# Kernel tuning notes

Measured on AMD Instinct MI355X. Metric: run time of the kernel, lower is better.

The kernel has to match this reference:

```python
import jax, jax.numpy as jnp
import numpy as np

NEG_SLOPE = 0.01  # torch LeakyReLU default

def setup_inputs() -> dict:
    key = jax.random.key(0)
    ks = jax.random.split(key, 8)
    B, T, D = 8, 2048, 512
    E, H = 8, 2 * D  # n_experts, ffn hidden
    s = 0.02
    return {
        "x":  jax.random.normal(ks[0], (B, T, D), dtype=jnp.float32),
        "Wr": jax.random.normal(ks[1], (D, E), dtype=jnp.float32) * s,
        "br": jnp.zeros((E,), dtype=jnp.float32),
        "W1": jax.random.normal(ks[2], (E, D, H), dtype=jnp.float32) * s,
        "b1": jnp.zeros((E, H), dtype=jnp.float32),
        "W2": jax.random.normal(ks[3], (E, H, D), dtype=jnp.float32) * s,
        "b2": jnp.zeros((E, D), dtype=jnp.float32),
    }

def reference(x, Wr, br, W1, b1, W2, b2):
    B, T, D = x.shape
    E = Wr.shape[1]
    top_k = 2
    balancing_coef = 1e-4
    x_flat = x.reshape(B * T, D)  # [N, D]

    # router: softmax over experts
    router_probs = jax.nn.softmax(x_flat @ Wr + br, axis=-1)  # [N, E]
    top_weights, top_indices = jax.lax.top_k(router_probs, top_k)  # [N, k]

    # dense all-expert FFN (faithful to original: every expert on every token)
    h = jax.nn.leaky_relu(jnp.einsum('nd,edh->neh', x_flat, W1) + b1, NEG_SLOPE)  # [N, E, H]
    expert_out = jax.nn.leaky_relu(jnp.einsum('neh,ehd->ned', h, W2) + b2, NEG_SLOPE)  # [N, E, D]
    # dropout is identity in eval mode

    # gather top-k expert outputs and combine with router weights
    top_out = jnp.take_along_axis(expert_out, top_indices[:, :, None], axis=1)  # [N, k, D]
    out_flat = jnp.sum(top_out * top_weights[:, :, None], axis=1)  # [N, D]
    output = out_flat.reshape(B, T, D)

    # load-balancing loss
    target = jnp.full((E,), 1.0 / E, dtype=x.dtype)
    mean_probs = jnp.mean(router_probs, axis=0)
    gating_loss = jnp.mean((target - mean_probs) ** 2) * balancing_coef
    return (output, gating_loss)
```

## Files before the change

### kernel.cpp

```cpp
#include <hip/hip_runtime.h>
#include <hip/hip_bf16.h>

constexpr int D_    = 512;
constexpr int H_    = 1024;
constexpr int E_    = 8;
constexpr int NTOK_ = 16384;
constexpr int MT_   = 64;
constexpr int NPAIR_= 2*NTOK_;
constexpr float NEG_ = 0.01f;

typedef short s16x8 __attribute__((ext_vector_type(8)));
typedef float f32x4 __attribute__((ext_vector_type(4)));

#define MFMA16(a,b,c) __builtin_amdgcn_mfma_f32_16x16x32_bf16((a),(b),(c),0,0,0)

__device__ __forceinline__ unsigned short f2bf(float f) {
  unsigned u = __float_as_uint(f);
  u += 0x7FFFu + ((u >> 16) & 1u);
  return (unsigned short)(u >> 16);
}
__device__ __forceinline__ float bf2f(unsigned u16) {
  return __uint_as_float(u16 << 16);
}
__device__ __forceinline__ float leaky(float v) {
  return v > 0.f ? v : NEG_ * v;
}

__global__ __launch_bounds__(256) void prep_kernel(
    const float* __restrict__ x, const float* __restrict__ Wr,
    const float* __restrict__ br,
    const float* __restrict__ W1, const float* __restrict__ W2,
    unsigned short* __restrict__ W1s, unsigned short* __restrict__ W2s,
    int* __restrict__ cnt, float* __restrict__ psum,
    int* __restrict__ tokE, int* __restrict__ tokSlot, float* __restrict__ tokW) {
  const int blk = blockIdx.x;
  const int tid = threadIdx.x;
  if (blk < 64) {
    __shared__ int lcnt[E_];
    __shared__ int gbase[E_];
    __shared__ float lp[E_];
    if (tid < E_) { lcnt[tid] = 0; lp[tid] = 0.f; }
    __syncthreads();

    int t = blk * 256 + tid;
    float acc[E_];
#pragma unroll
    for (int e = 0; e < E_; e++) acc[e] = br[e];
    const float4* xr = (const float4*)(x + (size_t)t * D_);
    for (int i = 0; i < D_ / 4; i++) {
      float4 v = xr[i];
      const float* w = Wr + (size_t)i * 4 * E_;
#pragma unroll
      for (int e = 0; e < E_; e++)
        acc[e] += v.x * w[e] + v.y * w[8 + e] + v.z * w[16 + e] + v.w * w[24 + e];
    }
    float mx = acc[0];
#pragma unroll
    for (int e = 1; e < E_; e++) mx = fmaxf(mx, acc[e]);
    float p[E_]; float s = 0.f;
#pragma unroll
    for (int e = 0; e < E_; e++) { p[e] = expf(acc[e] - mx); s += p[e]; }
    float inv = 1.f / s;
#pragma unroll
    for (int e = 0; e < E_; e++) p[e] *= inv;

    float m1 = -1.f, m2 = -1.f; int i1 = 0, i2 = 0;
#pragma unroll
    for (int e = 0; e < E_; e++) {
      float pe = p[e];
      if (pe > m1)      { m2 = m1; i2 = i1; m1 = pe; i1 = e; }
      else if (pe > m2) { m2 = pe; i2 = e; }
    }
    int s1 = atomicAdd(&lcnt[i1], 1);
    int s2 = atomicAdd(&lcnt[i2], 1);

#pragma unroll
    for (int e = 0; e < E_; e++) {
      float v = p[e];
#pragma unroll
      for (int o = 32; o > 0; o >>= 1) v += __shfl_xor(v, o);
      if ((tid & 63) == 0) atomicAdd(&lp[e], v);
    }
    __syncthreads();
    if (tid < E_) {
      gbase[tid] = atomicAdd(&cnt[tid * 16], lcnt[tid]);
      atomicAdd(&psum[tid * 16], lp[tid]);
    }
    __syncthreads();
    tokE[2 * t]     = i1; tokSlot[2 * t]     = gbase[i1] + s1; tokW[2 * t]     = m1;
    tokE[2 * t + 1] = i2; tokSlot[2 * t + 1] = gbase[i2] + s2; tokW[2 * t + 1] = m2;
  } else {
    int gid = (blk - 64) * 256 + tid;
    const int HALF = E_ * 64 * 16 * 64;
    if (gid < HALF) {
      int lane = gid & 63, kk = (gid >> 6) & 15, nt = (gid >> 10) & 63, e = gid >> 16;
      int k0 = kk * 32 + (lane >> 4) * 8;
      int n  = nt * 16 + (lane & 15);
      const float* src = W1 + ((size_t)(e * 512 + k0)) * 1024 + n;
      s16x8 v;
#pragma unroll
      for (int j = 0; j < 8; j++) v[j] = (short)f2bf(src[(size_t)j * 1024]);
      *(s16x8*)(W1s + (size_t)gid * 8) = v;
    } else {
      int c = gid - HALF;
      int lane = c & 63, kk = (c >> 6) & 31, nt = (c >> 11) & 31, e = c >> 16;
      int k0 = kk * 32 + (lane >> 4) * 8;
      int n  = nt * 16 + (lane & 15);
      const float* src = W2 + ((size_t)(e * 1024 + k0)) * 512 + n;
      s16x8 v;
#pragma unroll
      for (int j = 0; j < 8; j++) v[j] = (short)f2bf(src[(size_t)j * 512]);
      *(s16x8*)(W2s + (size_t)c * 8) = v;
    }
  }
}

__global__ __launch_bounds__(256) void assign_kernel(
    const int* __restrict__ tokE, const int* __restrict__ tokSlot,
    const int* __restrict__ cnt, const float* __restrict__ psum,
    int* __restrict__ posOfTok, int* __restrict__ tokOfPos,
    float* __restrict__ loss_out) {
  __shared__ int soff[E_];
  int tid = threadIdx.x;
  if (tid == 0) {
    int o = 0;
#pragma unroll
    for (int e = 0; e < E_; e++) { soff[e] = o; o += cnt[e * 16]; }
  }
  __syncthreads();
  int p = blockIdx.x * 256 + tid;
  int pos = soff[tokE[p]] + tokSlot[p];
  posOfTok[p] = pos;
  tokOfPos[pos] = p >> 1;
  if (blockIdx.x == 0 && tid == 0) {
    float l = 0.f;
#pragma unroll
    for (int e = 0; e < E_; e++) {
      float d = 0.125f - psum[e * 16] / (float)NTOK_;
      l += d * d;
    }
    *loss_out = (l / 8.f) * 1e-4f;
  }
}

__global__ __launch_bounds__(512, 2) void ffn_kernel(
    const float* __restrict__ x,
    const unsigned short* __restrict__ W1s, const unsigned short* __restrict__ W2s,
    const float* __restrict__ b1, const float* __restrict__ b2,
    const int* __restrict__ cnt, const int* __restrict__ tokOfPos,
    unsigned short* __restrict__ buf) {
  const int e = blockIdx.x & 7;
  const int tile = blockIdx.x >> 3;
  int nTok = 0, base0 = 0;
#pragma unroll
  for (int i = 0; i < E_; i++) {
    int ci = cnt[i * 16];
    if (i < e) base0 += ci;
    if (i == e) nTok = ci;
  }
  const int start = tile * MT_;
  if (start >= nTok) return;
  const int valid = min(MT_, nTok - start);
  const int base = base0 + start;

  __shared__ __align__(16) unsigned short xs[MT_][D_ + 8];
  __shared__ __align__(16) unsigned short hs[MT_][D_ + 8];

  const int tid = threadIdx.x;
  const int w = tid >> 6;
  const int lane = tid & 63;

  for (int r = w; r < MT_; r += 8) {
    int tok = tokOfPos[base + min(r, valid - 1)];
    const float4* src = (const float4*)(x + (size_t)tok * D_);
    float4 a = src[lane * 2], b = src[lane * 2 + 1];
    s16x8 v;
    v[0] = (short)f2bf(a.x); v[1] = (short)f2bf(a.y);
    v[2] = (short)f2bf(a.z); v[3] = (short)f2bf(a.w);
    v[4] = (short)f2bf(b.x); v[5] = (short)f2bf(b.y);
    v[6] = (short)f2bf(b.z); v[7] = (short)f2bf(b.w);
    *(s16x8*)&xs[r][lane * 8] = v;
  }
  __syncthreads();

  const int qm = lane & 15;
  const int qk = (lane >> 4) * 8;
  const int qr = (lane >> 4) * 4;

  f32x4 acc2[4][4];
#pragma unroll
  for (int mi = 0; mi < 4; mi++)
#pragma unroll
    for (int ni = 0; ni < 4; ni++) acc2[mi][ni] = {0.f, 0.f, 0.f, 0.f};

  const unsigned short* B1w = W1s + ((size_t)(e * 64 + w * 4) * 16) * 512 + lane * 8;
  const unsigned short* B2w = W2s + ((size_t)(e * 32 + w * 4) * 32) * 512 + lane * 8;

  for (int c = 0; c < 2; c++) {
    f32x4 acc1[4][4];
#pragma unroll
    for (int mi = 0; mi < 4; mi++)
#pragma unroll
      for (int ni = 0; ni < 4; ni++) acc1[mi][ni] = {0.f, 0.f, 0.f, 0.f};

    const unsigned short* B1c = B1w + (size_t)(c * 32 * 16) * 512;
#pragma unroll 4
    for (int kk = 0; kk < 16; kk++) {
      s16x8 bf[4], af[4];
#pragma unroll
      for (int ni = 0; ni < 4; ni++)
        bf[ni] = *(const s16x8*)(B1c + (size_t)(ni * 16 + kk) * 512);
#pragma unroll
      for (int mi = 0; mi < 4; mi++)
        af[mi] = *(const s16x8*)&xs[mi * 16 + qm][kk * 32 + qk];
#pragma unroll
      for (int ni = 0; ni < 4; ni++)
#pragma unroll
        for (int mi = 0; mi < 4; mi++)
          acc1[mi][ni] = MFMA16(af[mi], bf[ni], acc1[mi][ni]);
    }
    __syncthreads();
#pragma unroll
    for (int ni = 0; ni < 4; ni++) {
      int hcol = w * 64 + ni * 16 + qm;
      float bb = b1[e * H_ + c * 512 + hcol];
#pragma unroll
      for (int mi = 0; mi < 4; mi++)
#pragma unroll
        for (int r4 = 0; r4 < 4; r4++)
          hs[mi * 16 + qr + r4][hcol] = f2bf(leaky(acc1[mi][ni][r4] + bb));
    }
    __syncthreads();
    const unsigned short* B2c = B2w + (size_t)(c * 16) * 512;
#pragma unroll 4
    for (int kk = 0; kk < 16; kk++) {
      s16x8 bf[4], af[4];
#pragma unroll
      for (int ni = 0; ni < 4; ni++)
        bf[ni] = *(const s16x8*)(B2c + (size_t)(ni * 32 + kk) * 512);
#pragma unroll
      for (int mi = 0; mi < 4; mi++)
        af[mi] = *(const s16x8*)&hs[mi * 16 + qm][kk * 32 + qk];
#pragma unroll
      for (int ni = 0; ni < 4; ni++)
#pragma unroll
        for (int mi = 0; mi < 4; mi++)
          acc2[mi][ni] = MFMA16(af[mi], bf[ni], acc2[mi][ni]);
    }
  }

#pragma unroll
  for (int mi = 0; mi < 4; mi++) {
#pragma unroll
    for (int r4 = 0; r4 < 4; r4++) {
      int row = mi * 16 + qr + r4;
      if (row < valid) {
        size_t rowbase = (size_t)(base + row) * D_;
#pragma unroll
        for (int ni = 0; ni < 4; ni++) {
          int col = w * 64 + ni * 16 + qm;
          float v = leaky(acc2[mi][ni][r4] + b2[e * D_ + col]);
          buf[rowbase + col] = f2bf(v);
        }
      }
    }
  }
}

__global__ __launch_bounds__(256) void combine_kernel(
    const unsigned short* __restrict__ buf, const int* __restrict__ posOfTok,
    const float* __restrict__ tokW, float* __restrict__ out) {
  int t = blockIdx.x * 4 + (threadIdx.x >> 6);
  int lane = threadIdx.x & 63;
  int p0 = posOfTok[2 * t], p1 = posOfTok[2 * t + 1];
  float w0 = tokW[2 * t], w1 = tokW[2 * t + 1];
  uint4 u0 = ((const uint4*)(buf + (size_t)p0 * D_))[lane];
  uint4 u1 = ((const uint4*)(buf + (size_t)p1 * D_))[lane];
  float4 oA, oB;
  oA.x = w0 * bf2f(u0.x & 0xFFFFu) + w1 * bf2f(u1.x & 0xFFFFu);
  oA.y = w0 * bf2f(u0.x >> 16)     + w1 * bf2f(u1.x >> 16);
  oA.z = w0 * bf2f(u0.y & 0xFFFFu) + w1 * bf2f(u1.y & 0xFFFFu);
  oA.w = w0 * bf2f(u0.y >> 16)     + w1 * bf2f(u1.y >> 16);
  oB.x = w0 * bf2f(u0.z & 0xFFFFu) + w1 * bf2f(u1.z & 0xFFFFu);
  oB.y = w0 * bf2f(u0.z >> 16)     + w1 * bf2f(u1.z >> 16);
  oB.z = w0 * bf2f(u0.w & 0xFFFFu) + w1 * bf2f(u1.w & 0xFFFFu);
  oB.w = w0 * bf2f(u0.w >> 16)     + w1 * bf2f(u1.w >> 16);
  float4* dst = (float4*)(out + (size_t)t * D_);
  dst[lane * 2]     = oA;
  dst[lane * 2 + 1] = oB;
}

extern "C" void kernel_launch(void* const* d_in, const int* in_sizes, int n_in,
                              void* d_out, int out_size, void* d_ws, size_t ws_size,
                              hipStream_t stream) {
  const float* x  = (const float*)d_in[0];
  const float* Wr = (const float*)d_in[1];
  const float* br = (const float*)d_in[2];
  const float* W1 = (const float*)d_in[3];
  const float* b1 = (const float*)d_in[4];
  const float* W2 = (const float*)d_in[5];
  const float* b2 = (const float*)d_in[6];
  float* out = (float*)d_out;

  char* ws = (char*)d_ws;
  int*   cnt      = (int*)(ws + 0);
  float* psum     = (float*)(ws + 512);
  int*   tokE     = (int*)(ws + 4096);
  int*   tokSlot  = (int*)(ws + 4096 + 1 * 131072);
  float* tokW     = (float*)(ws + 4096 + 2 * 131072);
  int*   posOfTok = (int*)(ws + 4096 + 3 * 131072);
  int*   tokOfPos = (int*)(ws + 4096 + 4 * 131072);
  unsigned short* W1s = (unsigned short*)(ws + (1u << 20));
  unsigned short* W2s = (unsigned short*)(ws + (1u << 20) + 16777216u);
  unsigned short* buf = (unsigned short*)(ws + (1u << 20) + 33554432u);

  hipMemsetAsync(d_ws, 0, 2048, stream);
  prep_kernel<<<4160, 256, 0, stream>>>(x, Wr, br, W1, W2, W1s, W2s,
                                        cnt, psum, tokE, tokSlot, tokW);
  assign_kernel<<<NPAIR_ / 256, 256, 0, stream>>>(tokE, tokSlot, cnt, psum,
                                                  posOfTok, tokOfPos,
                                                  out + (size_t)NTOK_ * D_);
  ffn_kernel<<<(NTOK_ / MT_) * E_, 512, 0, stream>>>(x, W1s, W2s, b1, b2,
                                                     cnt, tokOfPos, buf);
  combine_kernel<<<NTOK_ / 4, 256, 0, stream>>>(buf, posOfTok, tokW, out);
}
```

Measured before the change: 298.4 us.

## Stage weight conversion through LDS and double-buffer MFMA operand loads

The weight pre-pack in prep_kernel now reads 64x64 fp32 tiles with coalesced float4 loads into shared memory and then transposes them into the MFMA-fragment bf16 layout. Before, each thread made eight strided scalar global reads. Separately, both GEMM loops in ffn_kernel now prefetch operands two k-steps ahead into register double buffers, and the bias loads and the first W2 fragments are hoisted ahead of the barrier. The aim is to hide global and LDS latency, at the cost of higher register pressure and a possible drop in occupancy.

```diff
diff --git a/kernel.cpp b/kernel.cpp
--- a/kernel.cpp
+++ b/kernel.cpp
@@ -90,27 +90,45 @@
     tokE[2 * t]     = i1; tokSlot[2 * t]     = gbase[i1] + s1; tokW[2 * t]     = m1;
     tokE[2 * t + 1] = i2; tokSlot[2 * t + 1] = gbase[i2] + s2; tokW[2 * t + 1] = m2;
   } else {
-    int gid = (blk - 64) * 256 + tid;
-    const int HALF = E_ * 64 * 16 * 64;
-    if (gid < HALF) {
-      int lane = gid & 63, kk = (gid >> 6) & 15, nt = (gid >> 10) & 63, e = gid >> 16;
-      int k0 = kk * 32 + (lane >> 4) * 8;
+    __shared__ float ldsf[64][68];
+    int bid = blk - 64;
+    const float* src;
+    int e, kt, tc, srcStride;
+    bool isW1 = bid < 1024;
+    if (isW1) {
+      e = bid >> 7; kt = (bid >> 4) & 7; tc = bid & 15; srcStride = 1024;
+      src = W1 + ((size_t)(e * 512 + kt * 64)) * 1024 + tc * 64;
+    } else {
+      int b2 = bid - 1024;
+      e = b2 >> 7; kt = (b2 >> 3) & 15; tc = b2 & 7; srcStride = 512;
+      src = W2 + ((size_t)(e * 1024 + kt * 64)) * 512 + tc * 64;
+    }
+#pragma unroll
+    for (int rep = 0; rep < 4; rep++) {
+      int row = rep * 16 + (tid >> 4);
+      int c4  = (tid & 15) * 4;
+      float4 v = *(const float4*)(src + (size_t)row * srcStride + c4);
+      ldsf[row][c4] = v.x; ldsf[row][c4 + 1] = v.y;
+      ldsf[row][c4 + 2] = v.z; ldsf[row][c4 + 3] = v.w;
+    }
+    __syncthreads();
+    int wv = tid >> 6, lane = tid & 63;
+#pragma unroll
+    for (int qi = 0; qi < 2; qi++) {
+      int q = wv * 2 + qi;
+      int ks = q >> 2, nt = q & 3;
+      int k0 = ks * 32 + (lane >> 4) * 8;
       int n  = nt * 16 + (lane & 15);
-      const float* src = W1 + ((size_t)(e * 512 + k0)) * 1024 + n;
       s16x8 v;
 #pragma unroll
-      for (int j = 0; j < 8; j++) v[j] = (short)f2bf(src[(size_t)j * 1024]);
-      *(s16x8*)(W1s + (size_t)gid * 8) = v;
-    } else {
-      int c = gid - HALF;
-      int lane = c & 63, kk = (c >> 6) & 31, nt = (c >> 11) & 31, e = c >> 16;
-      int k0 = kk * 32 + (lane >> 4) * 8;
-      int n  = nt * 16 + (lane & 15);
-      const float* src = W2 + ((size_t)(e * 1024 + k0)) * 512 + n;
-      s16x8 v;
-#pragma unroll
-      for (int j = 0; j < 8; j++) v[j] = (short)f2bf(src[(size_t)j * 512]);
-      *(s16x8*)(W2s + (size_t)c * 8) = v;
+      for (int j = 0; j < 8; j++) v[j] = (short)f2bf(ldsf[k0 + j][n]);
+      if (isW1) {
+        int ntg = tc * 4 + nt, kkg = kt * 2 + ks;
+        *(s16x8*)(W1s + (((size_t)e << 16) + (ntg << 10) + (kkg << 6) + lane) * 8) = v;
+      } else {
+        int ntg = tc * 4 + nt, kkg = kt * 2 + ks;
+        *(s16x8*)(W2s + (((size_t)e << 16) + (ntg << 11) + (kkg << 6) + lane) * 8) = v;
+      }
     }
   }
 }
@@ -204,48 +222,89 @@
       for (int ni = 0; ni < 4; ni++) acc1[mi][ni] = {0.f, 0.f, 0.f, 0.f};
 
     const unsigned short* B1c = B1w + (size_t)(c * 32 * 16) * 512;
-#pragma unroll 4
+    float bb[4];
+#pragma unroll
+    for (int ni = 0; ni < 4; ni++)
+      bb[ni] = b1[e * H_ + c * 512 + w * 64 + ni * 16 + qm];
+
+    s16x8 bfp[2][4], afp[2][4];
+#pragma unroll
+    for (int s = 0; s < 2; s++) {
+#pragma unroll
+      for (int ni = 0; ni < 4; ni++)
+        bfp[s][ni] = *(const s16x8*)(B1c + (size_t)(ni * 16 + s) * 512);
+#pragma unroll
+      for (int mi = 0; mi < 4; mi++)
+        afp[s][mi] = *(const s16x8*)&xs[mi * 16 + qm][s * 32 + qk];
+    }
+#pragma unroll
     for (int kk = 0; kk < 16; kk++) {
-      s16x8 bf[4], af[4];
+      s16x8 bcur[4], acur[4];
+#pragma unroll
+      for (int ni = 0; ni < 4; ni++) bcur[ni] = bfp[kk & 1][ni];
+#pragma unroll
+      for (int mi = 0; mi < 4; mi++) acur[mi] = afp[kk & 1][mi];
+      if (kk + 2 < 16) {
+#pragma unroll
+        for (int ni = 0; ni < 4; ni++)
+          bfp[kk & 1][ni] = *(const s16x8*)(B1c + (size_t)(ni * 16 + kk + 2) * 512);
+#pragma unroll
+        for (int mi = 0; mi < 4; mi++)
+          afp[kk & 1][mi] = *(const s16x8*)&xs[mi * 16 + qm][(kk + 2) * 32 + qk];
+      }
 #pragma unroll
       for (int ni = 0; ni < 4; ni++)
-        bf[ni] = *(const s16x8*)(B1c + (size_t)(ni * 16 + kk) * 512);
-#pragma unroll
-      for (int mi = 0; mi < 4; mi++)
-        af[mi] = *(const s16x8*)&xs[mi * 16 + qm][kk * 32 + qk];
+#pragma unroll
+        for (int mi = 0; mi < 4; mi++)
+          acc1[mi][ni] = MFMA16(acur[mi], bcur[ni], acc1[mi][ni]);
+    }
+    __syncthreads();
+
+    const unsigned short* B2c = B2w + (size_t)(c * 16) * 512;
+    s16x8 b2p[2][4];
+#pragma unroll
+    for (int s = 0; s < 2; s++)
 #pragma unroll
       for (int ni = 0; ni < 4; ni++)
-#pragma unroll
-        for (int mi = 0; mi < 4; mi++)
-          acc1[mi][ni] = MFMA16(af[mi], bf[ni], acc1[mi][ni]);
-    }
-    __syncthreads();
+        b2p[s][ni] = *(const s16x8*)(B2c + (size_t)(ni * 32 + s) * 512);
+
 #pragma unroll
     for (int ni = 0; ni < 4; ni++) {
       int hcol = w * 64 + ni * 16 + qm;
-      float bb = b1[e * H_ + c * 512 + hcol];
 #pragma unroll
       for (int mi = 0; mi < 4; mi++)
 #pragma unroll
         for (int r4 = 0; r4 < 4; r4++)
-          hs[mi * 16 + qr + r4][hcol] = f2bf(leaky(acc1[mi][ni][r4] + bb));
-    }
-    __syncthreads();
-    const unsigned short* B2c = B2w + (size_t)(c * 16) * 512;
-#pragma unroll 4
+          hs[mi * 16 + qr + r4][hcol] = f2bf(leaky(acc1[mi][ni][r4] + bb[ni]));
+    }
+    __syncthreads();
+
+    s16x8 a2p[2][4];
+#pragma unroll
+    for (int s = 0; s < 2; s++)
+#pragma unroll
+      for (int mi = 0; mi < 4; mi++)
+        a2p[s][mi] = *(const s16x8*)&hs[mi * 16 + qm][s * 32 + qk];
+#pragma unroll
     for (int kk = 0; kk < 16; kk++) {
-      s16x8 bf[4], af[4];
+      s16x8 bcur[4], acur[4];
+#pragma unroll
+      for (int ni = 0; ni < 4; ni++) bcur[ni] = b2p[kk & 1][ni];
+#pragma unroll
+      for (int mi = 0; mi < 4; mi++) acur[mi] = a2p[kk & 1][mi];
+      if (kk + 2 < 16) {
+#pragma unroll
+        for (int ni = 0; ni < 4; ni++)
+          b2p[kk & 1][ni] = *(const s16x8*)(B2c + (size_t)(ni * 32 + kk + 2) * 512);
+#pragma unroll
+        for (int mi = 0; mi < 4; mi++)
+          a2p[kk & 1][mi] = *(const s16x8*)&hs[mi * 16 + qm][(kk + 2) * 32 + qk];
+      }
 #pragma unroll
       for (int ni = 0; ni < 4; ni++)
-        bf[ni] = *(const s16x8*)(B2c + (size_t)(ni * 32 + kk) * 512);
-#pragma unroll
-      for (int mi = 0; mi < 4; mi++)
-        af[mi] = *(const s16x8*)&hs[mi * 16 + qm][kk * 32 + qk];
-#pragma unroll
-      for (int ni = 0; ni < 4; ni++)
 #pragma unroll
         for (int mi = 0; mi < 4; mi++)
-          acc2[mi][ni] = MFMA16(af[mi], bf[ni], acc2[mi][ni]);
+          acc2[mi][ni] = MFMA16(acur[mi], bcur[ni], acc2[mi][ni]);
     }
   }
 
@@ -315,8 +374,8 @@
   unsigned short* buf = (unsigned short*)(ws + (1u << 20) + 33554432u);
 
   hipMemsetAsync(d_ws, 0, 2048, stream);
-  prep_kernel<<<4160, 256, 0, stream>>>(x, Wr, br, W1, W2, W1s, W2s,
-                                        cnt, psum, tokE, tokSlot, tokW);
+  prep_kernel<<<64 + 2048, 256, 0, stream>>>(x, Wr, br, W1, W2, W1s, W2s,
+                                             cnt, psum, tokE, tokSlot, tokW);
   assign_kernel<<<NPAIR_ / 256, 256, 0, stream>>>(tokE, tokSlot, cnt, psum,
                                                   posOfTok, tokOfPos,
                                                   out + (size_t)NTOK_ * D_);
```

Result: no change. 295.1 us (-1.1%).
